# Kernel tuning notes

Measured on AMD Instinct MI355X. Metric: run time of the kernel, lower is better.

## Reference

```python
import jax, jax.numpy as jnp
import numpy as np

DIM = 128
EDGE_FEAT_DIM = 2
N_NODES = 50000
N_EDGES = 600000
EPS = 1e-5


def setup_inputs() -> dict:
    key = jax.random.key(0)
    ks = jax.random.split(key, 16)
    d = DIM
    inp = {}
    inp["x"] = jax.random.normal(ks[0], (N_NODES, d), dtype=jnp.float32)
    inp["edge_index"] = jax.random.randint(ks[1], (2, N_EDGES), 0, N_NODES, dtype=jnp.int32)
    inp["edge_weight_norm"] = jax.random.uniform(ks[2], (N_EDGES,), dtype=jnp.float32)
    inp["edge_feat"] = jax.random.normal(ks[3], (N_EDGES, EDGE_FEAT_DIM), dtype=jnp.float32)
    inp["batch"] = jnp.zeros((N_NODES,), dtype=jnp.int32)
    # phi: Linear(dim, dim)
    inp["W_phi"] = jax.random.normal(ks[4], (d, d), dtype=jnp.float32) * (1.0 / np.sqrt(d))
    inp["b_phi"] = jnp.zeros((d,), dtype=jnp.float32)
    # edge_gate: Linear(2d+2, d) -> BN(d) -> GELU -> Linear(d, 1)
    din = 2 * d + EDGE_FEAT_DIM
    inp["W_g1"] = jax.random.normal(ks[5], (din, d), dtype=jnp.float32) * (1.0 / np.sqrt(din))
    inp["b_g1"] = jnp.zeros((d,), dtype=jnp.float32)
    inp["bn_gamma"] = jnp.ones((d,), dtype=jnp.float32)
    inp["bn_beta"] = jnp.zeros((d,), dtype=jnp.float32)
    inp["bn_mean"] = jnp.zeros((d,), dtype=jnp.float32)
    inp["bn_var"] = jnp.ones((d,), dtype=jnp.float32)
    inp["W_g2"] = jax.random.normal(ks[6], (d, 1), dtype=jnp.float32) * (1.0 / np.sqrt(d))
    inp["b_g2"] = jnp.zeros((1,), dtype=jnp.float32)
    # upd: Linear(2d, d)
    inp["W_u"] = jax.random.normal(ks[7], (2 * d, d), dtype=jnp.float32) * (1.0 / np.sqrt(2 * d))
    inp["b_u"] = jnp.zeros((d,), dtype=jnp.float32)
    # LayerNorm(dim)
    inp["ln_gamma"] = jnp.ones((d,), dtype=jnp.float32)
    inp["ln_beta"] = jnp.zeros((d,), dtype=jnp.float32)
    return inp


def reference(x, edge_index, edge_weight_norm, edge_feat, batch,
              W_phi, b_phi, W_g1, b_g1, bn_gamma, bn_beta, bn_mean, bn_var,
              W_g2, b_g2, W_u, b_u, ln_gamma, ln_beta):
    src, dst = edge_index[0], edge_index[1]
    # phi(x): [N, d]
    xj = x @ W_phi + b_phi
    # edge gate MLP on [x_dst, x_src, e]: [E, 2d+2]
    g_in = jnp.concatenate([x[dst], x[src], edge_feat], axis=-1)
    h1 = g_in @ W_g1 + b_g1
    h1 = (h1 - bn_mean) * jax.lax.rsqrt(bn_var + EPS) * bn_gamma + bn_beta  # BN eval mode
    h1 = jax.nn.gelu(h1, approximate=False)
    gate = jax.nn.sigmoid(h1 @ W_g2 + b_g2)[:, 0]  # [E]
    # messages and scatter-add aggregation
    msg = xj[src] * (edge_weight_norm * gate)[:, None]  # [E, d]
    agg = jax.ops.segment_sum(msg, dst, num_segments=x.shape[0])  # [N, d]
    # update MLP + GELU + residual + LayerNorm
    h = jnp.concatenate([x, agg], axis=-1) @ W_u + b_u
    h = jax.nn.gelu(h, approximate=False)
    y = x + h
    mu = jnp.mean(y, axis=-1, keepdims=True)
    var = jnp.var(y, axis=-1, keepdims=True)
    return (y - mu) * jax.lax.rsqrt(var + EPS) * ln_gamma + ln_beta
```

## Files before the change

kernel.cpp:

```cpp
#include <hip/hip_runtime.h>
#include <hip/hip_fp16.h>
#include <math.h>

#define DIM 128
#define NN 50000
#define NE 600000
#define EPS 1e-5f
#define CAP 64

struct H8 { __half2 h[4]; };
struct F8 { float4 a, b; };

typedef _Float16 f16x8 __attribute__((ext_vector_type(8)));
typedef float    f32x4 __attribute__((ext_vector_type(4)));

__device__ __forceinline__ float gelu_fast(float x) {
    const float c1 = 2.3022085f;
    const float c2 = 0.1029437f;
    const float x2 = x * x;
    const float z  = x * __builtin_fmaf(c2, x2, c1);
    const float u  = __builtin_amdgcn_exp2f(z);
    const float r  = __builtin_amdgcn_rcpf(1.f + u);
    return __builtin_fmaf(-x, r, x);
}

__device__ __forceinline__ float sigmoid_fast(float y) {
    const float u = __builtin_amdgcn_exp2f(-1.4426950409f * y);
    return __builtin_amdgcn_rcpf(1.f + u);
}

__global__ __launch_bounds__(256) void k_prep_scale(
    const float* __restrict__ Wg1, const float* __restrict__ bg1,
    const float* __restrict__ bng, const float* __restrict__ bnb,
    const float* __restrict__ bnm, const float* __restrict__ bnv,
    __half* __restrict__ WABth, float* __restrict__ bA,
    float* __restrict__ w0p, float* __restrict__ w1p)
{
    const int k = blockIdx.x;
    const int t = threadIdx.x;
    const int c = t & 127;
    const float s = bng[c] * rsqrtf(bnv[c] + EPS);
    const float w = (t < 128) ? Wg1[k * DIM + c] : Wg1[(DIM + k) * DIM + c];
    WABth[t * DIM + k] = __float2half(w * s);
    if (k == 0 && t < 128) {
        const float tt = bnb[c] - bnm[c] * s;
        bA[c]  = bg1[c] * s + tt;
        w0p[c] = Wg1[256 * DIM + c] * s;
        w1p[c] = Wg1[257 * DIM + c] * s;
    }
}

__global__ __launch_bounds__(128) void k_prep_wpu(
    const float* __restrict__ Wphi, const float* __restrict__ bphi,
    const float* __restrict__ Wu,
    __half* __restrict__ Wct, float* __restrict__ bpu)
{
    const int a = blockIdx.x;
    const int j = threadIdx.x;
    float acc = 0.f;
    #pragma unroll 8
    for (int k = 0; k < DIM; ++k)
        acc += Wphi[a * DIM + k] * Wu[(DIM + k) * DIM + j];
    Wct[j * 256 + a]       = __float2half(Wu[a * DIM + j]);
    Wct[j * 256 + 128 + a] = __float2half(acc);
    if (a == 0) {
        float b = 0.f;
        #pragma unroll 8
        for (int k = 0; k < DIM; ++k)
            b += bphi[k] * Wu[(DIM + k) * DIM + j];
        bpu[j] = b;
    }
}

__global__ __launch_bounds__(256) void k_node_mfma(
    const float* __restrict__ x, const __half* __restrict__ WABth,
    const float* __restrict__ bA,
    __half* __restrict__ A, __half* __restrict__ Bv, __half* __restrict__ xh)
{
    __shared__ __half tile[64][264];
    const int t    = threadIdx.x;
    const int wv   = t >> 6;
    const int lane = t & 63;
    const int n16  = lane & 15;
    const int quad = lane >> 4;
    const int m0   = blockIdx.x * 64;

    f32x4 acc[4][4];
    #pragma unroll
    for (int mt = 0; mt < 4; ++mt)
        #pragma unroll
        for (int nt = 0; nt < 4; ++nt)
            acc[mt][nt] = (f32x4){0.f, 0.f, 0.f, 0.f};

    int rowm[4];
    #pragma unroll
    for (int mt = 0; mt < 4; ++mt)
        rowm[mt] = min(m0 + mt * 16 + n16, NN - 1);

    #pragma unroll
    for (int ks = 0; ks < 4; ++ks) {
        const int ko = ks * 32 + quad * 8;
        f16x8 bf[4];
        #pragma unroll
        for (int nt = 0; nt < 4; ++nt) {
            const int c = wv * 64 + nt * 16 + n16;
            bf[nt] = *(const f16x8*)(WABth + c * DIM + ko);
        }
        #pragma unroll
        for (int mt = 0; mt < 4; ++mt) {
            const float4 xa = *(const float4*)(x + (size_t)rowm[mt] * DIM + ko);
            const float4 xb = *(const float4*)(x + (size_t)rowm[mt] * DIM + ko + 4);
            f16x8 af;
            af[0] = (_Float16)xa.x; af[1] = (_Float16)xa.y;
            af[2] = (_Float16)xa.z; af[3] = (_Float16)xa.w;
            af[4] = (_Float16)xb.x; af[5] = (_Float16)xb.y;
            af[6] = (_Float16)xb.z; af[7] = (_Float16)xb.w;
            if (wv == 0)
                *(f16x8*)(xh + (size_t)rowm[mt] * DIM + ko) = af;
            #pragma unroll
            for (int nt = 0; nt < 4; ++nt)
                acc[mt][nt] = __builtin_amdgcn_mfma_f32_16x16x32_f16(
                    af, bf[nt], acc[mt][nt], 0, 0, 0);
        }
    }

    #pragma unroll
    for (int nt = 0; nt < 4; ++nt) {
        const int c = wv * 64 + nt * 16 + n16;
        const float bias = (c < 128) ? bA[c] : 0.f;
        #pragma unroll
        for (int mt = 0; mt < 4; ++mt)
            #pragma unroll
            for (int reg = 0; reg < 4; ++reg)
                tile[mt * 16 + quad * 4 + reg][c] =
                    __float2half(acc[mt][nt][reg] + bias);
    }
    __syncthreads();

    #pragma unroll
    for (int i = 0; i < 8; ++i) {
        const int chunk = t + i * 256;
        const int row = chunk >> 5;
        const int o   = (chunk & 31) * 8;
        if (m0 + row < NN) {
            const uint4 v = *(const uint4*)&tile[row][o];
            if (o < 128) *(uint4*)(A  + (size_t)(m0 + row) * DIM + o)       = v;
            else         *(uint4*)(Bv + (size_t)(m0 + row) * DIM + o - 128) = v;
        }
    }
}

__global__ __launch_bounds__(256) void k_gate(
    const int*   __restrict__ ei,  const float* __restrict__ ew,
    const float* __restrict__ ef,
    const __half* __restrict__ A,  const __half* __restrict__ Bv,
    const float* __restrict__ w0p, const float* __restrict__ w1p,
    const float* __restrict__ Wg2, const float* __restrict__ bg2,
    int* __restrict__ deg, int2* __restrict__ pairs)
{
    const int t    = threadIdx.x;
    const int lane = t & 63;
    const int sub  = lane >> 4;
    const int sl   = lane & 15;
    const int c8   = sl * 8;
    const int e0   = (blockIdx.x * 4 + (t >> 6)) * 8 + sub * 2;

    const F8 WG = *(const F8*)(Wg2 + c8);
    const F8 W0 = *(const F8*)(w0p + c8);
    const F8 W1 = *(const F8*)(w1p + c8);
    const float bg2v = bg2[0];
    const float* w0 = (const float*)&W0;
    const float* w1 = (const float*)&W1;
    const float* wg = (const float*)&WG;

    const int2   srcs = *(const int2*)(ei + e0);
    const int2   dsts = *(const int2*)(ei + NE + e0);
    const float4 efv  = *(const float4*)(ef + 2 * e0);
    const float2 ewv  = *(const float2*)(ew + e0);

    const H8 a0 = *(const H8*)(A  + (size_t)dsts.x * DIM + c8);
    const H8 b0 = *(const H8*)(Bv + (size_t)srcs.x * DIM + c8);
    const H8 a1 = *(const H8*)(A  + (size_t)dsts.y * DIM + c8);
    const H8 b1 = *(const H8*)(Bv + (size_t)srcs.y * DIM + c8);

    float p0 = 0.f, p1 = 0.f;
    #pragma unroll
    for (int i = 0; i < 4; ++i) {
        const float2 s0 = __half22float2(__hadd2(a0.h[i], b0.h[i]));
        const float2 s1 = __half22float2(__hadd2(a1.h[i], b1.h[i]));
        const int c0 = 2 * i, c1 = 2 * i + 1;
        float h;
        h = s0.x + efv.x * w0[c0] + efv.y * w1[c0];
        p0 = __builtin_fmaf(gelu_fast(h), wg[c0], p0);
        h = s0.y + efv.x * w0[c1] + efv.y * w1[c1];
        p0 = __builtin_fmaf(gelu_fast(h), wg[c1], p0);
        h = s1.x + efv.z * w0[c0] + efv.w * w1[c0];
        p1 = __builtin_fmaf(gelu_fast(h), wg[c0], p1);
        h = s1.y + efv.z * w0[c1] + efv.w * w1[c1];
        p1 = __builtin_fmaf(gelu_fast(h), wg[c1], p1);
    }
    #pragma unroll
    for (int off = 1; off < 16; off <<= 1) {
        p0 += __shfl_xor(p0, off, 64);
        p1 += __shfl_xor(p1, off, 64);
    }

    if (sl == 0) {
        const float coef0 = ewv.x * sigmoid_fast(p0 + bg2v);
        const float coef1 = ewv.y * sigmoid_fast(p1 + bg2v);
        const int pos0 = atomicAdd(&deg[dsts.x], 1);
        if (pos0 < CAP)
            pairs[(size_t)dsts.x * CAP + pos0] = make_int2(srcs.x, __float_as_int(coef0));
        const int pos1 = atomicAdd(&deg[dsts.y], 1);
        if (pos1 < CAP)
            pairs[(size_t)dsts.y * CAP + pos1] = make_int2(srcs.y, __float_as_int(coef1));
    }
}

__global__ __launch_bounds__(128, 3) void k_agg_update(
    const int* __restrict__ deg, const int2* __restrict__ pairs,
    const __half* __restrict__ xh, const __half* __restrict__ Wct,
    const float* __restrict__ bu, const float* __restrict__ bpu,
    const float* __restrict__ lng, const float* __restrict__ lnb,
    float* __restrict__ out)
{
    __shared__ __half xt[16][136];
    __shared__ __half at[2][16][136];
    __shared__ float  sct[2][16];
    __shared__ float  sred_s[2][16];
    __shared__ float  sred_ss[2][16];

    const int t    = threadIdx.x;
    const int w    = t >> 6;
    const int lane = t & 63;
    const int n16  = lane & 15;
    const int quad = lane >> 4;
    const int m0   = blockIdx.x * 16;

    const int slot = quad;
    const int sl   = n16;
    const int c8   = sl * 8;

    int    cnt[4];
    size_t pb[4];
    #pragma unroll
    for (int r = 0; r < 4; ++r) {
        const int lr = r * 4 + slot;
        const int nc = min(m0 + lr, NN - 1);
        const int d  = min(deg[nc], CAP);
        const int h  = ((d + 2) >> 2) << 1;
        const int lo = w ? h : 0;
        const int hi = w ? d : h;
        cnt[r] = hi - lo;
        pb[r]  = (size_t)nc * CAP + lo;
    }

    #pragma unroll
    for (int i = 0; i < 2; ++i) {
        const int idx = i * 128 + t;
        const int row = idx >> 4;
        const int col = (idx & 15) * 8;
        const int grow = min(m0 + row, NN - 1);
        *(f16x8*)&xt[row][col] = *(const f16x8*)(xh + (size_t)grow * DIM + col);
    }

    float acc[4][8];
    float scn[4] = {0.f, 0.f, 0.f, 0.f};
    #pragma unroll
    for (int r = 0; r < 4; ++r)
        #pragma unroll
        for (int i = 0; i < 8; ++i) acc[r][i] = 0.f;

    const int cmax = max(max(cnt[0], cnt[1]), max(cnt[2], cnt[3]));

    for (int jj = 0; jj < cmax; jj += 4) {
        int4 pq0[4], pq1[4];
        #pragma unroll
        for (int r = 0; r < 4; ++r) {
            pq0[r] = *(const int4*)(&pairs[pb[r] + jj]);
            pq1[r] = *(const int4*)(&pairs[pb[r] + jj + 2]);
        }

        int   ix[16];
        float cf[16];
        #pragma unroll
        for (int r = 0; r < 4; ++r) {
            const int q = 4 * r;
            const bool v0 = (jj     < cnt[r]);
            const bool v1 = (jj + 1 < cnt[r]);
            const bool v2 = (jj + 2 < cnt[r]);
            const bool v3 = (jj + 3 < cnt[r]);
            ix[q]     = v0 ? pq0[r].x : 0;
            cf[q]     = v0 ? __int_as_float(pq0[r].y) : 0.f;
            ix[q + 1] = v1 ? pq0[r].z : 0;
            cf[q + 1] = v1 ? __int_as_float(pq0[r].w) : 0.f;
            ix[q + 2] = v2 ? pq1[r].x : 0;
            cf[q + 2] = v2 ? __int_as_float(pq1[r].y) : 0.f;
            ix[q + 3] = v3 ? pq1[r].z : 0;
            cf[q + 3] = v3 ? __int_as_float(pq1[r].w) : 0.f;
        }

        H8 xv[16];
        #pragma unroll
        for (int q = 0; q < 16; ++q)
            xv[q] = *(const H8*)(xh + (size_t)ix[q] * DIM + c8);

        #pragma unroll
        for (int r = 0; r < 4; ++r) {
            #pragma unroll
            for (int k = 0; k < 4; ++k) {
                const int   q = 4 * r + k;
                const float c = cf[q];
                #pragma unroll
                for (int i = 0; i < 4; ++i) {
                    const float2 f = __half22float2(xv[q].h[i]);
                    acc[r][2 * i]     = __builtin_fmaf(c, f.x, acc[r][2 * i]);
                    acc[r][2 * i + 1] = __builtin_fmaf(c, f.y, acc[r][2 * i + 1]);
                }
                scn[r] += c;
            }
        }
    }

    #pragma unroll
    for (int r = 0; r < 4; ++r) {
        const int lr = r * 4 + slot;
        f16x8 hv;
        #pragma unroll
        for (int i = 0; i < 8; ++i) hv[i] = (_Float16)acc[r][i];
        *(f16x8*)&at[w][lr][c8] = hv;
        if (sl == 0) sct[w][lr] = scn[r];
    }
    __syncthreads();

    f32x4 acc2[4];
    #pragma unroll
    for (int nt = 0; nt < 4; ++nt) acc2[nt] = (f32x4){0.f, 0.f, 0.f, 0.f};

    const int rloc = n16;
    #pragma unroll
    for (int ks = 0; ks < 4; ++ks) {
        const int ko = ks * 32 + quad * 8;
        const f16x8 af = *(const f16x8*)&xt[rloc][ko];
        #pragma unroll
        for (int nt = 0; nt < 4; ++nt) {
            const int c = w * 64 + nt * 16 + n16;
            const f16x8 bf = *(const f16x8*)(Wct + c * 256 + ko);
            acc2[nt] = __builtin_amdgcn_mfma_f32_16x16x32_f16(af, bf, acc2[nt], 0, 0, 0);
        }
    }
    #pragma unroll
    for (int half = 0; half < 2; ++half) {
        #pragma unroll
        for (int ks = 0; ks < 4; ++ks) {
            const int ko = ks * 32 + quad * 8;
            const f16x8 af = *(const f16x8*)&at[half][rloc][ko];
            #pragma unroll
            for (int nt = 0; nt < 4; ++nt) {
                const int c = w * 64 + nt * 16 + n16;
                const f16x8 bf = *(const f16x8*)(Wct + c * 256 + 128 + ko);
                acc2[nt] = __builtin_amdgcn_mfma_f32_16x16x32_f16(af, bf, acc2[nt], 0, 0, 0);
            }
        }
    }

    int   rl[4];
    float scv[4];
    #pragma unroll
    for (int reg = 0; reg < 4; ++reg) {
        rl[reg]  = quad * 4 + reg;
        scv[reg] = sct[0][rl[reg]] + sct[1][rl[reg]];
    }

    float yv[4][4];
    float s[4]  = {0.f, 0.f, 0.f, 0.f};
    float ss[4] = {0.f, 0.f, 0.f, 0.f};

    #pragma unroll
    for (int nt = 0; nt < 4; ++nt) {
        const int c = w * 64 + nt * 16 + n16;
        const float buv = bu[c], bpv = bpu[c];
        #pragma unroll
        for (int reg = 0; reg < 4; ++reg) {
            float h = acc2[nt][reg] + buv + scv[reg] * bpv;
            h = gelu_fast(h);
            const float xv = __half2float(xt[rl[reg]][c]);
            const float y = xv + h;
            yv[nt][reg] = y;
            s[reg]  += y;
            ss[reg] += y * y;
        }
    }

    #pragma unroll
    for (int reg = 0; reg < 4; ++reg) {
        #pragma unroll
        for (int off = 1; off < 16; off <<= 1) {
            s[reg]  += __shfl_xor(s[reg],  off, 64);
            ss[reg] += __shfl_xor(ss[reg], off, 64);
        }
    }
    if (n16 == 0) {
        #pragma unroll
        for (int reg = 0; reg < 4; ++reg) {
            sred_s[w][rl[reg]]  = s[reg];
            sred_ss[w][rl[reg]] = ss[reg];
        }
    }
    __syncthreads();

    float mu[4], rs[4];
    #pragma unroll
    for (int reg = 0; reg < 4; ++reg) {
        const float stot  = sred_s[0][rl[reg]]  + sred_s[1][rl[reg]];
        const float sstot = sred_ss[0][rl[reg]] + sred_ss[1][rl[reg]];
        mu[reg] = stot * (1.f / DIM);
        const float var = sstot * (1.f / DIM) - mu[reg] * mu[reg];
        rs[reg] = rsqrtf(var + EPS);
    }

    #pragma unroll
    for (int nt = 0; nt < 4; ++nt) {
        const int c = w * 64 + nt * 16 + n16;
        const float gg = lng[c], bb2 = lnb[c];
        #pragma unroll
        for (int reg = 0; reg < 4; ++reg) {
            const int grow = m0 + rl[reg];
            if (grow < NN)
                __builtin_nontemporal_store(
                    (yv[nt][reg] - mu[reg]) * rs[reg] * gg + bb2,
                    &out[(size_t)grow * DIM + c]);
        }
    }
}

extern "C" void kernel_launch(void* const* d_in, const int* in_sizes, int n_in,
                              void* d_out, int out_size, void* d_ws, size_t ws_size,
                              hipStream_t stream)
{
    const float* x    = (const float*)d_in[0];
    const int*   ei   = (const int*)  d_in[1];
    const float* ew   = (const float*)d_in[2];
    const float* ef   = (const float*)d_in[3];
    const float* Wphi = (const float*)d_in[5];
    const float* bphi = (const float*)d_in[6];
    const float* Wg1  = (const float*)d_in[7];
    const float* bg1  = (const float*)d_in[8];
    const float* bng  = (const float*)d_in[9];
    const float* bnb  = (const float*)d_in[10];
    const float* bnm  = (const float*)d_in[11];
    const float* bnv  = (const float*)d_in[12];
    const float* Wg2  = (const float*)d_in[13];
    const float* bg2  = (const float*)d_in[14];
    const float* Wu   = (const float*)d_in[15];
    const float* bu   = (const float*)d_in[16];
    const float* lng  = (const float*)d_in[17];
    const float* lnb  = (const float*)d_in[18];

    float* out = (float*)d_out;

    char* wsb = (char*)d_ws;
    size_t off = 0;
    auto carve = [&](size_t bytes) -> void* {
        void* p = wsb + off;
        off += (bytes + 255) & ~(size_t)255;
        return p;
    };
    __half* xh    = (__half*)carve((size_t)NN * DIM * 2);
    __half* A     = (__half*)carve((size_t)NN * DIM * 2);
    __half* Bv    = (__half*)carve((size_t)NN * DIM * 2);
    __half* WABth = (__half*)carve(256 * DIM * 2);
    __half* Wct   = (__half*)carve(DIM * 256 * 2);
    float*  bA    = (float*) carve(DIM * 4);
    float*  w0p   = (float*) carve(DIM * 4);
    float*  w1p   = (float*) carve(DIM * 4);
    float*  bpu   = (float*) carve(DIM * 4);
    int*    deg   = (int*)   carve((size_t)NN * 4);
    int2*   pairs = (int2*)  carve((size_t)NN * CAP * 8 + 256);

    hipMemsetAsync(deg, 0, (size_t)NN * 4, stream);

    k_prep_scale<<<128, 256, 0, stream>>>(Wg1, bg1, bng, bnb, bnm, bnv,
                                          WABth, bA, w0p, w1p);
    k_prep_wpu<<<128, 128, 0, stream>>>(Wphi, bphi, Wu, Wct, bpu);
    k_node_mfma<<<(NN + 63) / 64, 256, 0, stream>>>(x, WABth, bA, A, Bv, xh);
    k_gate<<<NE / 32, 256, 0, stream>>>(ei, ew, ef, A, Bv, w0p, w1p, Wg2, bg2,
                                        deg, pairs);
    k_agg_update<<<(NN + 15) / 16, 128, 0, stream>>>(deg, pairs, xh, Wct,
                                                     bu, bpu, lng, lnb, out);
}
```

Measured before the change: 269.3 us.

## Fuse edge gate into aggregation and bucket edges inside node kernel

Drops the separate gate kernel. Edge bucketing by destination now runs as extra blocks of the node GEMM kernel and stores packed records: src index with quantized edge weight, plus half-precision edge features. The gate MLP is then computed inside the aggregation kernel per destination row, reusing the destination's A row, while Bv and xh are interleaved into one BX buffer so a single gather fetches both. This removes a kernel launch and a pass over the A/Bv gathers, at the cost of 15-bit edge-weight quantization and fp16 edge features that reduce accuracy, plus more compute inside the latency-bound aggregation loop.

```diff
diff --git a/kernel.cpp b/kernel.cpp
--- a/kernel.cpp
+++ b/kernel.cpp
@@ -7,6 +7,8 @@
 #define NE 600000
 #define EPS 1e-5f
 #define CAP 64
+#define NB_NODE 782
+#define NB_EDGE 586
 
 struct H8 { __half2 h[4]; };
 struct F8 { float4 a, b; };
@@ -72,12 +74,38 @@
     }
 }
 
-__global__ __launch_bounds__(256) void k_node_mfma(
+__global__ __launch_bounds__(256) void k_node_bucket(
     const float* __restrict__ x, const __half* __restrict__ WABth,
     const float* __restrict__ bA,
-    __half* __restrict__ A, __half* __restrict__ Bv, __half* __restrict__ xh)
+    const int* __restrict__ ei, const float* __restrict__ ew,
+    const float* __restrict__ ef,
+    __half* __restrict__ A, __half* __restrict__ BX,
+    int* __restrict__ deg, int2* __restrict__ rec)
 {
     __shared__ __half tile[64][264];
+
+    if (blockIdx.x >= NB_NODE) {
+        const int tid = (blockIdx.x - NB_NODE) * 256 + threadIdx.x;
+        #pragma unroll
+        for (int k = 0; k < 4; ++k) {
+            const int e = tid + k * (NB_EDGE * 256);
+            if (e < NE) {
+                const int s = ei[e];
+                const int d = ei[NE + e];
+                const float2 efv = *(const float2*)(ef + 2 * e);
+                const int ewq = (int)fminf(ew[e] * 32768.f + 0.5f, 32767.f);
+                int2 r;
+                r.x = s | (ewq << 17);
+                r.y = (int)__half_as_ushort(__float2half(efv.x)) |
+                      ((int)__half_as_ushort(__float2half(efv.y)) << 16);
+                const int pos = atomicAdd(&deg[d], 1);
+                if (pos < CAP)
+                    rec[(size_t)d * CAP + pos] = r;
+            }
+        }
+        return;
+    }
+
     const int t    = threadIdx.x;
     const int wv   = t >> 6;
     const int lane = t & 63;
@@ -116,7 +144,7 @@
             af[4] = (_Float16)xb.x; af[5] = (_Float16)xb.y;
             af[6] = (_Float16)xb.z; af[7] = (_Float16)xb.w;
             if (wv == 0)
-                *(f16x8*)(xh + (size_t)rowm[mt] * DIM + ko) = af;
+                *(f16x8*)(BX + (size_t)rowm[mt] * 256 + 2 * ko + 8) = af;
             #pragma unroll
             for (int nt = 0; nt < 4; ++nt)
                 acc[mt][nt] = __builtin_amdgcn_mfma_f32_16x16x32_f16(
@@ -144,82 +172,20 @@
         const int o   = (chunk & 31) * 8;
         if (m0 + row < NN) {
             const uint4 v = *(const uint4*)&tile[row][o];
-            if (o < 128) *(uint4*)(A  + (size_t)(m0 + row) * DIM + o)       = v;
-            else         *(uint4*)(Bv + (size_t)(m0 + row) * DIM + o - 128) = v;
-        }
-    }
-}
-
-__global__ __launch_bounds__(256) void k_gate(
-    const int*   __restrict__ ei,  const float* __restrict__ ew,
-    const float* __restrict__ ef,
-    const __half* __restrict__ A,  const __half* __restrict__ Bv,
+            if (o < 128)
+                *(uint4*)(A + (size_t)(m0 + row) * DIM + o) = v;
+            else
+                *(uint4*)(BX + (size_t)(m0 + row) * 256 + 2 * (o - 128)) = v;
+        }
+    }
+}
+
+__global__ __launch_bounds__(128, 3) void k_agg_update(
+    const int* __restrict__ deg, const int2* __restrict__ rec,
+    const __half* __restrict__ A, const __half* __restrict__ BX,
+    const __half* __restrict__ Wct,
     const float* __restrict__ w0p, const float* __restrict__ w1p,
     const float* __restrict__ Wg2, const float* __restrict__ bg2,
-    int* __restrict__ deg, int2* __restrict__ pairs)
-{
-    const int t    = threadIdx.x;
-    const int lane = t & 63;
-    const int sub  = lane >> 4;
-    const int sl   = lane & 15;
-    const int c8   = sl * 8;
-    const int e0   = (blockIdx.x * 4 + (t >> 6)) * 8 + sub * 2;
-
-    const F8 WG = *(const F8*)(Wg2 + c8);
-    const F8 W0 = *(const F8*)(w0p + c8);
-    const F8 W1 = *(const F8*)(w1p + c8);
-    const float bg2v = bg2[0];
-    const float* w0 = (const float*)&W0;
-    const float* w1 = (const float*)&W1;
-    const float* wg = (const float*)&WG;
-
-    const int2   srcs = *(const int2*)(ei + e0);
-    const int2   dsts = *(const int2*)(ei + NE + e0);
-    const float4 efv  = *(const float4*)(ef + 2 * e0);
-    const float2 ewv  = *(const float2*)(ew + e0);
-
-    const H8 a0 = *(const H8*)(A  + (size_t)dsts.x * DIM + c8);
-    const H8 b0 = *(const H8*)(Bv + (size_t)srcs.x * DIM + c8);
-    const H8 a1 = *(const H8*)(A  + (size_t)dsts.y * DIM + c8);
-    const H8 b1 = *(const H8*)(Bv + (size_t)srcs.y * DIM + c8);
-
-    float p0 = 0.f, p1 = 0.f;
-    #pragma unroll
-    for (int i = 0; i < 4; ++i) {
-        const float2 s0 = __half22float2(__hadd2(a0.h[i], b0.h[i]));
-        const float2 s1 = __half22float2(__hadd2(a1.h[i], b1.h[i]));
-        const int c0 = 2 * i, c1 = 2 * i + 1;
-        float h;
-        h = s0.x + efv.x * w0[c0] + efv.y * w1[c0];
-        p0 = __builtin_fmaf(gelu_fast(h), wg[c0], p0);
-        h = s0.y + efv.x * w0[c1] + efv.y * w1[c1];
-        p0 = __builtin_fmaf(gelu_fast(h), wg[c1], p0);
-        h = s1.x + efv.z * w0[c0] + efv.w * w1[c0];
-        p1 = __builtin_fmaf(gelu_fast(h), wg[c0], p1);
-        h = s1.y + efv.z * w0[c1] + efv.w * w1[c1];
-        p1 = __builtin_fmaf(gelu_fast(h), wg[c1], p1);
-    }
-    #pragma unroll
-    for (int off = 1; off < 16; off <<= 1) {
-        p0 += __shfl_xor(p0, off, 64);
-        p1 += __shfl_xor(p1, off, 64);
-    }
-
-    if (sl == 0) {
-        const float coef0 = ewv.x * sigmoid_fast(p0 + bg2v);
-        const float coef1 = ewv.y * sigmoid_fast(p1 + bg2v);
-        const int pos0 = atomicAdd(&deg[dsts.x], 1);
-        if (pos0 < CAP)
-            pairs[(size_t)dsts.x * CAP + pos0] = make_int2(srcs.x, __float_as_int(coef0));
-        const int pos1 = atomicAdd(&deg[dsts.y], 1);
-        if (pos1 < CAP)
-            pairs[(size_t)dsts.y * CAP + pos1] = make_int2(srcs.y, __float_as_int(coef1));
-    }
-}
-
-__global__ __launch_bounds__(128, 3) void k_agg_update(
-    const int* __restrict__ deg, const int2* __restrict__ pairs,
-    const __half* __restrict__ xh, const __half* __restrict__ Wct,
     const float* __restrict__ bu, const float* __restrict__ bpu,
     const float* __restrict__ lng, const float* __restrict__ lnb,
     float* __restrict__ out)
@@ -243,6 +209,7 @@
 
     int    cnt[4];
     size_t pb[4];
+    H8     arow[4];
     #pragma unroll
     for (int r = 0; r < 4; ++r) {
         const int lr = r * 4 + slot;
@@ -253,15 +220,25 @@
         const int hi = w ? d : h;
         cnt[r] = hi - lo;
         pb[r]  = (size_t)nc * CAP + lo;
-    }
+        arow[r] = *(const H8*)(A + (size_t)nc * DIM + c8);
+    }
+
+    const F8 W0 = *(const F8*)(w0p + c8);
+    const F8 W1 = *(const F8*)(w1p + c8);
+    const F8 WG = *(const F8*)(Wg2 + c8);
+    const float bg2v = bg2[0];
+    const float* w0 = (const float*)&W0;
+    const float* w1 = (const float*)&W1;
+    const float* wg = (const float*)&WG;
 
     #pragma unroll
     for (int i = 0; i < 2; ++i) {
         const int idx = i * 128 + t;
         const int row = idx >> 4;
-        const int col = (idx & 15) * 8;
+        const int cb  = idx & 15;
         const int grow = min(m0 + row, NN - 1);
-        *(f16x8*)&xt[row][col] = *(const f16x8*)(xh + (size_t)grow * DIM + col);
+        *(f16x8*)&xt[row][cb * 8] =
+            *(const f16x8*)(BX + (size_t)grow * 256 + cb * 16 + 8);
     }
 
     float acc[4][8];
@@ -273,52 +250,58 @@
 
     const int cmax = max(max(cnt[0], cnt[1]), max(cnt[2], cnt[3]));
 
-    for (int jj = 0; jj < cmax; jj += 4) {
-        int4 pq0[4], pq1[4];
+    for (int jj = 0; jj < cmax; jj += 2) {
         #pragma unroll
         for (int r = 0; r < 4; ++r) {
-            pq0[r] = *(const int4*)(&pairs[pb[r] + jj]);
-            pq1[r] = *(const int4*)(&pairs[pb[r] + jj + 2]);
-        }
-
-        int   ix[16];
-        float cf[16];
-        #pragma unroll
-        for (int r = 0; r < 4; ++r) {
-            const int q = 4 * r;
+            const int4 pq = *(const int4*)(&rec[pb[r] + jj]);
             const bool v0 = (jj     < cnt[r]);
             const bool v1 = (jj + 1 < cnt[r]);
-            const bool v2 = (jj + 2 < cnt[r]);
-            const bool v3 = (jj + 3 < cnt[r]);
-            ix[q]     = v0 ? pq0[r].x : 0;
-            cf[q]     = v0 ? __int_as_float(pq0[r].y) : 0.f;
-            ix[q + 1] = v1 ? pq0[r].z : 0;
-            cf[q + 1] = v1 ? __int_as_float(pq0[r].w) : 0.f;
-            ix[q + 2] = v2 ? pq1[r].x : 0;
-            cf[q + 2] = v2 ? __int_as_float(pq1[r].y) : 0.f;
-            ix[q + 3] = v3 ? pq1[r].z : 0;
-            cf[q + 3] = v3 ? __int_as_float(pq1[r].w) : 0.f;
-        }
-
-        H8 xv[16];
-        #pragma unroll
-        for (int q = 0; q < 16; ++q)
-            xv[q] = *(const H8*)(xh + (size_t)ix[q] * DIM + c8);
-
-        #pragma unroll
-        for (int r = 0; r < 4; ++r) {
-            #pragma unroll
-            for (int k = 0; k < 4; ++k) {
-                const int   q = 4 * r + k;
-                const float c = cf[q];
-                #pragma unroll
-                for (int i = 0; i < 4; ++i) {
-                    const float2 f = __half22float2(xv[q].h[i]);
-                    acc[r][2 * i]     = __builtin_fmaf(c, f.x, acc[r][2 * i]);
-                    acc[r][2 * i + 1] = __builtin_fmaf(c, f.y, acc[r][2 * i + 1]);
-                }
-                scn[r] += c;
+            const int sx0 = v0 ? (pq.x & 0x1FFFF) : 0;
+            const int sx1 = v1 ? (pq.z & 0x1FFFF) : 0;
+            const float ew0 = v0 ? (float)((unsigned)pq.x >> 17) * (1.f/32768.f) : 0.f;
+            const float ew1 = v1 ? (float)((unsigned)pq.z >> 17) * (1.f/32768.f) : 0.f;
+            const float2 ef0 = __half22float2(*(const __half2*)&pq.y);
+            const float2 ef1 = __half22float2(*(const __half2*)&pq.w);
+
+            const H8 bv0 = *(const H8*)(BX + (size_t)sx0 * 256 + sl * 16);
+            const H8 xv0 = *(const H8*)(BX + (size_t)sx0 * 256 + sl * 16 + 8);
+            const H8 bv1 = *(const H8*)(BX + (size_t)sx1 * 256 + sl * 16);
+            const H8 xv1 = *(const H8*)(BX + (size_t)sx1 * 256 + sl * 16 + 8);
+
+            float p0 = 0.f, p1 = 0.f;
+            #pragma unroll
+            for (int i = 0; i < 4; ++i) {
+                const float2 s0 = __half22float2(__hadd2(arow[r].h[i], bv0.h[i]));
+                const float2 s1 = __half22float2(__hadd2(arow[r].h[i], bv1.h[i]));
+                const int c0 = 2 * i, c1 = 2 * i + 1;
+                float h;
+                h = s0.x + ef0.x * w0[c0] + ef0.y * w1[c0];
+                p0 = __builtin_fmaf(gelu_fast(h), wg[c0], p0);
+                h = s0.y + ef0.x * w0[c1] + ef0.y * w1[c1];
+                p0 = __builtin_fmaf(gelu_fast(h), wg[c1], p0);
+                h = s1.x + ef1.x * w0[c0] + ef1.y * w1[c0];
+                p1 = __builtin_fmaf(gelu_fast(h), wg[c0], p1);
+                h = s1.y + ef1.x * w0[c1] + ef1.y * w1[c1];
+                p1 = __builtin_fmaf(gelu_fast(h), wg[c1], p1);
             }
+            #pragma unroll
+            for (int off = 1; off < 16; off <<= 1) {
+                p0 += __shfl_xor(p0, off, 64);
+                p1 += __shfl_xor(p1, off, 64);
+            }
+            const float coef0 = ew0 * sigmoid_fast(p0 + bg2v);
+            const float coef1 = ew1 * sigmoid_fast(p1 + bg2v);
+
+            #pragma unroll
+            for (int i = 0; i < 4; ++i) {
+                const float2 f0 = __half22float2(xv0.h[i]);
+                const float2 f1 = __half22float2(xv1.h[i]);
+                acc[r][2 * i]     = __builtin_fmaf(coef0, f0.x, acc[r][2 * i]);
+                acc[r][2 * i + 1] = __builtin_fmaf(coef0, f0.y, acc[r][2 * i + 1]);
+                acc[r][2 * i]     = __builtin_fmaf(coef1, f1.x, acc[r][2 * i]);
+                acc[r][2 * i + 1] = __builtin_fmaf(coef1, f1.y, acc[r][2 * i + 1]);
+            }
+            scn[r] += coef0 + coef1;
         }
     }
 
@@ -466,9 +449,8 @@
         off += (bytes + 255) & ~(size_t)255;
         return p;
     };
-    __half* xh    = (__half*)carve((size_t)NN * DIM * 2);
     __half* A     = (__half*)carve((size_t)NN * DIM * 2);
-    __half* Bv    = (__half*)carve((size_t)NN * DIM * 2);
+    __half* BX    = (__half*)carve((size_t)NN * 256 * 2);
     __half* WABth = (__half*)carve(256 * DIM * 2);
     __half* Wct   = (__half*)carve(DIM * 256 * 2);
     float*  bA    = (float*) carve(DIM * 4);
@@ -476,16 +458,16 @@
     float*  w1p   = (float*) carve(DIM * 4);
     float*  bpu   = (float*) carve(DIM * 4);
     int*    deg   = (int*)   carve((size_t)NN * 4);
-    int2*   pairs = (int2*)  carve((size_t)NN * CAP * 8 + 256);
+    int2*   rec   = (int2*)  carve((size_t)NN * CAP * 8 + 256);
 
     hipMemsetAsync(deg, 0, (size_t)NN * 4, stream);
 
     k_prep_scale<<<128, 256, 0, stream>>>(Wg1, bg1, bng, bnb, bnm, bnv,
                                           WABth, bA, w0p, w1p);
     k_prep_wpu<<<128, 128, 0, stream>>>(Wphi, bphi, Wu, Wct, bpu);
-    k_node_mfma<<<(NN + 63) / 64, 256, 0, stream>>>(x, WABth, bA, A, Bv, xh);
-    k_gate<<<NE / 32, 256, 0, stream>>>(ei, ew, ef, A, Bv, w0p, w1p, Wg2, bg2,
-                                        deg, pairs);
-    k_agg_update<<<(NN + 15) / 16, 128, 0, stream>>>(deg, pairs, xh, Wct,
-                                                     bu, bpu, lng, lnb, out);
-}
+    k_node_bucket<<<NB_NODE + NB_EDGE, 256, 0, stream>>>(
+        x, WABth, bA, ei, ew, ef, A, BX, deg, rec);
+    k_agg_update<<<(NN + 15) / 16, 128, 0, stream>>>(
+        deg, rec, A, BX, Wct, w0p, w1p, Wg2, bg2,
+        bu, bpu, lng, lnb, out);
+}
```

Result: slower. 293.2 us (+8.9%).

## Bucket edges by destination before gating and compute gate per destination node

Applied to the files above, without the earlier changes.

Edges are now bucketed by destination (packed src, quantized weight, fp16 edge features) in extra blocks appended to the node GEMM launch. A new per-node gate kernel then loads the destination's A row once, gathers only source rows, and writes the gate coefficient back into the record buffer. This removes the random A gathers and overlaps the bucketing atomics with the node GEMM. In exchange it quantizes edge weights to 15 bits and edge features to fp16. It also launches one 256-thread block per node, where most waves exit early.

```diff
diff --git a/kernel.cpp b/kernel.cpp
--- a/kernel.cpp
+++ b/kernel.cpp
@@ -7,6 +7,8 @@
 #define NE 600000
 #define EPS 1e-5f
 #define CAP 64
+#define NB_NODE 782
+#define NB_EDGE 586
 
 struct H8 { __half2 h[4]; };
 struct F8 { float4 a, b; };
@@ -72,12 +74,38 @@
     }
 }
 
-__global__ __launch_bounds__(256) void k_node_mfma(
+__global__ __launch_bounds__(256) void k_node_bucket(
     const float* __restrict__ x, const __half* __restrict__ WABth,
     const float* __restrict__ bA,
-    __half* __restrict__ A, __half* __restrict__ Bv, __half* __restrict__ xh)
+    const int* __restrict__ ei, const float* __restrict__ ew,
+    const float* __restrict__ ef,
+    __half* __restrict__ A, __half* __restrict__ Bv, __half* __restrict__ xh,
+    int* __restrict__ deg, int2* __restrict__ rec)
 {
     __shared__ __half tile[64][264];
+
+    if (blockIdx.x >= NB_NODE) {
+        const int tid = (blockIdx.x - NB_NODE) * 256 + threadIdx.x;
+        #pragma unroll
+        for (int k = 0; k < 4; ++k) {
+            const int e = tid + k * (NB_EDGE * 256);
+            if (e < NE) {
+                const int s = ei[e];
+                const int d = ei[NE + e];
+                const float2 efv = *(const float2*)(ef + 2 * e);
+                const int ewq = (int)fminf(ew[e] * 32768.f + 0.5f, 32767.f);
+                int2 r;
+                r.x = s | (ewq << 17);
+                r.y = (int)__half_as_ushort(__float2half(efv.x)) |
+                      ((int)__half_as_ushort(__float2half(efv.y)) << 16);
+                const int pos = atomicAdd(&deg[d], 1);
+                if (pos < CAP)
+                    rec[(size_t)d * CAP + pos] = r;
+            }
+        }
+        return;
+    }
+
     const int t    = threadIdx.x;
     const int wv   = t >> 6;
     const int lane = t & 63;
@@ -150,75 +178,85 @@
     }
 }
 
-__global__ __launch_bounds__(256) void k_gate(
-    const int*   __restrict__ ei,  const float* __restrict__ ew,
-    const float* __restrict__ ef,
-    const __half* __restrict__ A,  const __half* __restrict__ Bv,
+__global__ __launch_bounds__(256) void k_gate2(
+    const int* __restrict__ deg, int2* __restrict__ rec,
+    const __half* __restrict__ A, const __half* __restrict__ Bv,
     const float* __restrict__ w0p, const float* __restrict__ w1p,
-    const float* __restrict__ Wg2, const float* __restrict__ bg2,
-    int* __restrict__ deg, int2* __restrict__ pairs)
+    const float* __restrict__ Wg2, const float* __restrict__ bg2)
 {
+    const int n = blockIdx.x;
+    const int d = min(deg[n], CAP);
     const int t    = threadIdx.x;
+    const int wv   = t >> 6;
+    if (16 * wv >= d) return;
+
     const int lane = t & 63;
     const int sub  = lane >> 4;
     const int sl   = lane & 15;
     const int c8   = sl * 8;
-    const int e0   = (blockIdx.x * 4 + (t >> 6)) * 8 + sub * 2;
-
-    const F8 WG = *(const F8*)(Wg2 + c8);
+    const int e0   = (4 * wv + sub) * 4;
+
+    const H8 ar = *(const H8*)(A + (size_t)n * DIM + c8);
+
     const F8 W0 = *(const F8*)(w0p + c8);
     const F8 W1 = *(const F8*)(w1p + c8);
+    const F8 WG = *(const F8*)(Wg2 + c8);
     const float bg2v = bg2[0];
     const float* w0 = (const float*)&W0;
     const float* w1 = (const float*)&W1;
     const float* wg = (const float*)&WG;
 
-    const int2   srcs = *(const int2*)(ei + e0);
-    const int2   dsts = *(const int2*)(ei + NE + e0);
-    const float4 efv  = *(const float4*)(ef + 2 * e0);
-    const float2 ewv  = *(const float2*)(ew + e0);
-
-    const H8 a0 = *(const H8*)(A  + (size_t)dsts.x * DIM + c8);
-    const H8 b0 = *(const H8*)(Bv + (size_t)srcs.x * DIM + c8);
-    const H8 a1 = *(const H8*)(A  + (size_t)dsts.y * DIM + c8);
-    const H8 b1 = *(const H8*)(Bv + (size_t)srcs.y * DIM + c8);
-
-    float p0 = 0.f, p1 = 0.f;
-    #pragma unroll
-    for (int i = 0; i < 4; ++i) {
-        const float2 s0 = __half22float2(__hadd2(a0.h[i], b0.h[i]));
-        const float2 s1 = __half22float2(__hadd2(a1.h[i], b1.h[i]));
-        const int c0 = 2 * i, c1 = 2 * i + 1;
-        float h;
-        h = s0.x + efv.x * w0[c0] + efv.y * w1[c0];
-        p0 = __builtin_fmaf(gelu_fast(h), wg[c0], p0);
-        h = s0.y + efv.x * w0[c1] + efv.y * w1[c1];
-        p0 = __builtin_fmaf(gelu_fast(h), wg[c1], p0);
-        h = s1.x + efv.z * w0[c0] + efv.w * w1[c0];
-        p1 = __builtin_fmaf(gelu_fast(h), wg[c0], p1);
-        h = s1.y + efv.z * w0[c1] + efv.w * w1[c1];
-        p1 = __builtin_fmaf(gelu_fast(h), wg[c1], p1);
-    }
-    #pragma unroll
-    for (int off = 1; off < 16; off <<= 1) {
-        p0 += __shfl_xor(p0, off, 64);
-        p1 += __shfl_xor(p1, off, 64);
-    }
-
-    if (sl == 0) {
-        const float coef0 = ewv.x * sigmoid_fast(p0 + bg2v);
-        const float coef1 = ewv.y * sigmoid_fast(p1 + bg2v);
-        const int pos0 = atomicAdd(&deg[dsts.x], 1);
-        if (pos0 < CAP)
-            pairs[(size_t)dsts.x * CAP + pos0] = make_int2(srcs.x, __float_as_int(coef0));
-        const int pos1 = atomicAdd(&deg[dsts.y], 1);
-        if (pos1 < CAP)
-            pairs[(size_t)dsts.y * CAP + pos1] = make_int2(srcs.y, __float_as_int(coef1));
+    const size_t base = (size_t)n * CAP;
+
+    #pragma unroll
+    for (int s = 0; s < 2; ++s) {
+        const int j0 = e0 + 2 * s;
+        if (j0 >= d) break;
+        const bool v1 = (j0 + 1 < d);
+
+        const int4 pq = *(const int4*)(&rec[base + j0]);
+        const int sx0 = pq.x & 0x1FFFF;
+        const int sx1 = v1 ? (pq.z & 0x1FFFF) : 0;
+        const float ew0 = (float)((unsigned)pq.x >> 17) * (1.f / 32768.f);
+        const float ew1 = v1 ? (float)((unsigned)pq.z >> 17) * (1.f / 32768.f) : 0.f;
+        const float2 ef0 = __half22float2(*(const __half2*)&pq.y);
+        const float2 ef1 = __half22float2(*(const __half2*)&pq.w);
+
+        const H8 b0 = *(const H8*)(Bv + (size_t)sx0 * DIM + c8);
+        const H8 b1 = *(const H8*)(Bv + (size_t)sx1 * DIM + c8);
+
+        float p0 = 0.f, p1 = 0.f;
+        #pragma unroll
+        for (int i = 0; i < 4; ++i) {
+            const float2 s0 = __half22float2(__hadd2(ar.h[i], b0.h[i]));
+            const float2 s1 = __half22float2(__hadd2(ar.h[i], b1.h[i]));
+            const int c0 = 2 * i, c1 = 2 * i + 1;
+            float h;
+            h = s0.x + ef0.x * w0[c0] + ef0.y * w1[c0];
+            p0 = __builtin_fmaf(gelu_fast(h), wg[c0], p0);
+            h = s0.y + ef0.x * w0[c1] + ef0.y * w1[c1];
+            p0 = __builtin_fmaf(gelu_fast(h), wg[c1], p0);
+            h = s1.x + ef1.x * w0[c0] + ef1.y * w1[c0];
+            p1 = __builtin_fmaf(gelu_fast(h), wg[c0], p1);
+            h = s1.y + ef1.x * w0[c1] + ef1.y * w1[c1];
+            p1 = __builtin_fmaf(gelu_fast(h), wg[c1], p1);
+        }
+        #pragma unroll
+        for (int off = 1; off < 16; off <<= 1) {
+            p0 += __shfl_xor(p0, off, 64);
+            p1 += __shfl_xor(p1, off, 64);
+        }
+
+        if (sl == 0) {
+            rec[base + j0].y = __float_as_int(ew0 * sigmoid_fast(p0 + bg2v));
+            if (v1)
+                rec[base + j0 + 1].y = __float_as_int(ew1 * sigmoid_fast(p1 + bg2v));
+        }
     }
 }
 
 __global__ __launch_bounds__(128, 3) void k_agg_update(
-    const int* __restrict__ deg, const int2* __restrict__ pairs,
+    const int* __restrict__ deg, const int2* __restrict__ rec,
     const __half* __restrict__ xh, const __half* __restrict__ Wct,
     const float* __restrict__ bu, const float* __restrict__ bpu,
     const float* __restrict__ lng, const float* __restrict__ lnb,
@@ -277,8 +315,8 @@
         int4 pq0[4], pq1[4];
         #pragma unroll
         for (int r = 0; r < 4; ++r) {
-            pq0[r] = *(const int4*)(&pairs[pb[r] + jj]);
-            pq1[r] = *(const int4*)(&pairs[pb[r] + jj + 2]);
+            pq0[r] = *(const int4*)(&rec[pb[r] + jj]);
+            pq1[r] = *(const int4*)(&rec[pb[r] + jj + 2]);
         }
 
         int   ix[16];
@@ -290,13 +328,13 @@
             const bool v1 = (jj + 1 < cnt[r]);
             const bool v2 = (jj + 2 < cnt[r]);
             const bool v3 = (jj + 3 < cnt[r]);
-            ix[q]     = v0 ? pq0[r].x : 0;
+            ix[q]     = v0 ? (pq0[r].x & 0x1FFFF) : 0;
             cf[q]     = v0 ? __int_as_float(pq0[r].y) : 0.f;
-            ix[q + 1] = v1 ? pq0[r].z : 0;
+            ix[q + 1] = v1 ? (pq0[r].z & 0x1FFFF) : 0;
             cf[q + 1] = v1 ? __int_as_float(pq0[r].w) : 0.f;
-            ix[q + 2] = v2 ? pq1[r].x : 0;
+            ix[q + 2] = v2 ? (pq1[r].x & 0x1FFFF) : 0;
             cf[q + 2] = v2 ? __int_as_float(pq1[r].y) : 0.f;
-            ix[q + 3] = v3 ? pq1[r].z : 0;
+            ix[q + 3] = v3 ? (pq1[r].z & 0x1FFFF) : 0;
             cf[q + 3] = v3 ? __int_as_float(pq1[r].w) : 0.f;
         }
 
@@ -476,16 +514,16 @@
     float*  w1p   = (float*) carve(DIM * 4);
     float*  bpu   = (float*) carve(DIM * 4);
     int*    deg   = (int*)   carve((size_t)NN * 4);
-    int2*   pairs = (int2*)  carve((size_t)NN * CAP * 8 + 256);
+    int2*   rec   = (int2*)  carve((size_t)NN * CAP * 8 + 256);
 
     hipMemsetAsync(deg, 0, (size_t)NN * 4, stream);
 
     k_prep_scale<<<128, 256, 0, stream>>>(Wg1, bg1, bng, bnb, bnm, bnv,
                                           WABth, bA, w0p, w1p);
     k_prep_wpu<<<128, 128, 0, stream>>>(Wphi, bphi, Wu, Wct, bpu);
-    k_node_mfma<<<(NN + 63) / 64, 256, 0, stream>>>(x, WABth, bA, A, Bv, xh);
-    k_gate<<<NE / 32, 256, 0, stream>>>(ei, ew, ef, A, Bv, w0p, w1p, Wg2, bg2,
-                                        deg, pairs);
-    k_agg_update<<<(NN + 15) / 16, 128, 0, stream>>>(deg, pairs, xh, Wct,
+    k_node_bucket<<<NB_NODE + NB_EDGE, 256, 0, stream>>>(
+        x, WABth, bA, ei, ew, ef, A, Bv, xh, deg, rec);
+    k_gate2<<<NN, 256, 0, stream>>>(deg, rec, A, Bv, w0p, w1p, Wg2, bg2);
+    k_agg_update<<<(NN + 15) / 16, 128, 0, stream>>>(deg, rec, xh, Wct,
                                                      bu, bpu, lng, lnb, out);
 }
```

After: 293.0 us. 8.8% more time.
